# Optimization experiments

Measured on AMD Instinct MI355X. Metric: run time of the kernel, lower is better.

Reference implementation:

```python
import jax, jax.numpy as jnp
import numpy as np

N = 50000      # nodes
E = 800000     # directed edges
D = 128        # input_dim == hidden_dim
EL = 100000    # edges scored by decoder


def setup_inputs() -> dict:
    key = jax.random.key(0)
    ks = jax.random.split(key, 8)
    s = 1.0 / np.sqrt(D)  # glorot-ish scale
    return {
        "node_feature": jax.random.normal(ks[0], (N, D), jnp.float32),
        "W1": jax.random.normal(ks[1], (D, D), jnp.float32) * s,
        "b1": jnp.zeros((D,), jnp.float32),
        "W2": jax.random.normal(ks[2], (D, D), jnp.float32) * s,
        "b2": jnp.zeros((D,), jnp.float32),
        "W3": jax.random.normal(ks[3], (D, D), jnp.float32) * s,
        "b3": jnp.zeros((D,), jnp.float32),
        "edge_index": jax.random.randint(ks[4], (2, E), 0, N, dtype=jnp.int32),
        "edge_label_index": jax.random.randint(ks[5], (2, EL), 0, N, dtype=jnp.int32),
    }


def _gcn_conv(x, W, b, src, dst, norm, n):
    # x' = D^{-1/2} (A + I) D^{-1/2} (x W) + b   (PyG GCNConv semantics)
    h = x @ W                                   # [N, D]
    msg = h[src] * norm[:, None]                # gather + scale, [E+N, D]
    out = jax.ops.segment_sum(msg, dst, num_segments=n)  # scatter-add
    return out + b


def reference(node_feature, W1, b1, W2, b2, W3, b3, edge_index, edge_label_index):
    n = node_feature.shape[0]
    loop = jnp.arange(n, dtype=edge_index.dtype)
    src = jnp.concatenate([edge_index[0], loop])  # self-loops appended
    dst = jnp.concatenate([edge_index[1], loop])
    # symmetric normalization: deg over destinations (incl. self-loops)
    deg = jax.ops.segment_sum(jnp.ones_like(dst, dtype=node_feature.dtype), dst, num_segments=n)
    dinv = jax.lax.rsqrt(jnp.maximum(deg, 1.0))
    norm = dinv[src] * dinv[dst]                 # [E+N]

    x = jax.nn.relu(_gcn_conv(node_feature, W1, b1, src, dst, norm, n))
    x = jax.nn.relu(_gcn_conv(x, W2, b2, src, dst, norm, n))
    x = _gcn_conv(x, W3, b3, src, dst, norm, n)

    # dot-product edge decoder
    u = x[edge_label_index[0]]
    v = x[edge_label_index[1]]
    return jnp.sum(u * v, axis=-1)               # [EL] logits
```

## Files before the change

kernel.cpp:

```cpp
#include <hip/hip_runtime.h>
#include <hip/hip_bf16.h>
#include <hip/hip_fp16.h>

typedef _Float16 v8h __attribute__((ext_vector_type(8)));
typedef float v4f __attribute__((ext_vector_type(4)));

__global__ __launch_bounds__(256) void gemm1_deg(const float* __restrict__ X,
                                                 const float* __restrict__ W,
                                                 __half* __restrict__ H, int Nrows,
                                                 int gemmBlocks, int degBlocks,
                                                 const int* __restrict__ dst,
                                                 int* __restrict__ cnt,
                                                 int* __restrict__ rank, int E,
                                                 const float* __restrict__ W2,
                                                 const float* __restrict__ W3,
                                                 __half* __restrict__ wfrag) {
    int tid = threadIdx.x;
    if (blockIdx.x >= gemmBlocks + degBlocks) {
        int o = (blockIdx.x - gemmBlocks - degBlocks) * 256 + tid;
        int w = o >> 14, r = o & 16383;
        const float* Ws = w ? W3 : W2;
        int k = r >> 7, ncol = r & 127;
        int c = ncol >> 4, nl = ncol & 15;
        int s = k >> 5, quad = (k >> 3) & 3, j = k & 7;
        int di = ((c * 4 + s) * 64 + quad * 16 + nl) * 8 + j;
        wfrag[(size_t)w * 16384 + di] = __float2half_rn(Ws[r]);
        return;
    }
    if (blockIdx.x >= gemmBlocks) {
        int base = (blockIdx.x - gemmBlocks) * 1024 + tid * 4;
        if (base + 3 < E) {
            int d0 = dst[base], d1 = dst[base + 1], d2 = dst[base + 2], d3 = dst[base + 3];
            int r0 = atomicAdd(&cnt[d0], 1);
            int r1 = atomicAdd(&cnt[d1], 1);
            int r2 = atomicAdd(&cnt[d2], 1);
            int r3 = atomicAdd(&cnt[d3], 1);
            rank[base] = r0; rank[base + 1] = r1; rank[base + 2] = r2; rank[base + 3] = r3;
        } else {
            for (int e = base; e < E; ++e) rank[e] = atomicAdd(&cnt[dst[e]], 1);
        }
        return;
    }
    __shared__ __align__(16) float xs[16][132];
    __shared__ __align__(16) float ws[16][128];
    int tx = tid & 15;
    int ty = tid >> 4;
    int row0 = blockIdx.x * 128;
    float acc[8][8] = {};
    for (int k0 = 0; k0 < 128; k0 += 16) {
        {
            int r = tid >> 2;
            int j = (tid & 3) * 4;
            int gr = row0 + r;
            float4 v = (gr < Nrows) ? *(const float4*)&X[(size_t)gr * 128 + k0 + j]
                                    : make_float4(0.f, 0.f, 0.f, 0.f);
            xs[j + 0][r] = v.x; xs[j + 1][r] = v.y; xs[j + 2][r] = v.z; xs[j + 3][r] = v.w;
            int gr2 = gr + 64;
            float4 u = (gr2 < Nrows) ? *(const float4*)&X[(size_t)gr2 * 128 + k0 + j]
                                     : make_float4(0.f, 0.f, 0.f, 0.f);
            xs[j + 0][r + 64] = u.x; xs[j + 1][r + 64] = u.y;
            xs[j + 2][r + 64] = u.z; xs[j + 3][r + 64] = u.w;
        }
        {
            const float4* Wv = (const float4*)&W[(size_t)k0 * 128];
            float4* wsv = (float4*)&ws[0][0];
            wsv[tid] = Wv[tid];
            wsv[tid + 256] = Wv[tid + 256];
        }
        __syncthreads();
#pragma unroll
        for (int kk = 0; kk < 16; ++kk) {
            float4 xa = *(float4*)&xs[kk][ty * 4];
            float4 xb = *(float4*)&xs[kk][ty * 4 + 64];
            float4 wa = *(float4*)&ws[kk][tx * 4];
            float4 wb = *(float4*)&ws[kk][tx * 4 + 64];
            float xr[8] = {xa.x, xa.y, xa.z, xa.w, xb.x, xb.y, xb.z, xb.w};
            float wr[8] = {wa.x, wa.y, wa.z, wa.w, wb.x, wb.y, wb.z, wb.w};
#pragma unroll
            for (int i = 0; i < 8; ++i)
#pragma unroll
                for (int j = 0; j < 8; ++j)
                    acc[i][j] += xr[i] * wr[j];
        }
        __syncthreads();
    }
    auto pk = [](float x, float y) { __half2 h = __floats2half2_rn(x, y); return *(unsigned int*)&h; };
#pragma unroll
    for (int i = 0; i < 8; ++i) {
        int gr = row0 + ((i < 4) ? (ty * 4 + i) : (64 + ty * 4 + i - 4));
        if (gr < Nrows) {
            uint2 q0 = make_uint2(pk(acc[i][0], acc[i][1]), pk(acc[i][2], acc[i][3]));
            uint2 q1 = make_uint2(pk(acc[i][4], acc[i][5]), pk(acc[i][6], acc[i][7]));
            *(uint2*)&H[(size_t)gr * 128 + tx * 4] = q0;
            *(uint2*)&H[(size_t)gr * 128 + 64 + tx * 4] = q1;
        }
    }
}

__global__ __launch_bounds__(256) void agg_gemm(const __half* __restrict__ Xs,
                                                const float* __restrict__ dinv,
                                                const int* __restrict__ rowptr,
                                                const int* __restrict__ col,
                                                const __half* __restrict__ wfrag,
                                                const float* __restrict__ bias,
                                                __half* __restrict__ Out,
                                                int n, int finalLayer) {
    __shared__ __align__(16) _Float16 y[64][136];
    int tid = threadIdx.x;
    int rowbase = blockIdx.x * 64;
    {
        int sub = tid >> 4;
        int t = (tid & 15) * 8;
        for (int g = 0; g < 4; ++g) {
            int rr = g * 16 + sub;
            int node = rowbase + rr;
            float a[8] = {};
            if (node < n) {
                int beg = rowptr[node], end = rowptr[node + 1];
                int k = beg;
                for (; k + 4 <= end; k += 4) {
                    int s0 = col[k], s1 = col[k + 1], s2 = col[k + 2], s3 = col[k + 3];
                    uint4 r0 = *(const uint4*)&Xs[(size_t)s0 * 128 + t];
                    uint4 r1 = *(const uint4*)&Xs[(size_t)s1 * 128 + t];
                    uint4 r2 = *(const uint4*)&Xs[(size_t)s2 * 128 + t];
                    uint4 r3 = *(const uint4*)&Xs[(size_t)s3 * 128 + t];
                    const __half2* h0 = (const __half2*)&r0;
                    const __half2* h1 = (const __half2*)&r1;
                    const __half2* h2 = (const __half2*)&r2;
                    const __half2* h3 = (const __half2*)&r3;
#pragma unroll
                    for (int m = 0; m < 4; ++m) {
                        float2 f0 = __half22float2(h0[m]);
                        float2 f1 = __half22float2(h1[m]);
                        float2 f2 = __half22float2(h2[m]);
                        float2 f3 = __half22float2(h3[m]);
                        a[2 * m]     += (f0.x + f1.x) + (f2.x + f3.x);
                        a[2 * m + 1] += (f0.y + f1.y) + (f2.y + f3.y);
                    }
                }
                for (; k < end; ++k) {
                    uint4 r0 = *(const uint4*)&Xs[(size_t)col[k] * 128 + t];
                    const __half2* h0 = (const __half2*)&r0;
#pragma unroll
                    for (int m = 0; m < 4; ++m) {
                        float2 f0 = __half22float2(h0[m]);
                        a[2 * m] += f0.x;
                        a[2 * m + 1] += f0.y;
                    }
                }
                float dn = dinv[node];
#pragma unroll
                for (int m = 0; m < 8; ++m) a[m] *= dn;
            }
            v8h yv;
#pragma unroll
            for (int m = 0; m < 8; ++m) yv[m] = (_Float16)a[m];
            *(v8h*)&y[rr][t] = yv;
        }
    }
    __syncthreads();
    int l = tid & 63;
    int wid = tid >> 6;
    int rb = wid * 16;
    int quad = l >> 4;
    int nn = l & 15;
    v8h a0 = *(const v8h*)&y[rb + nn][0 * 32 + quad * 8];
    v8h a1 = *(const v8h*)&y[rb + nn][1 * 32 + quad * 8];
    v8h a2 = *(const v8h*)&y[rb + nn][2 * 32 + quad * 8];
    v8h a3 = *(const v8h*)&y[rb + nn][3 * 32 + quad * 8];
    const v8h* Wf = (const v8h*)wfrag;
    v4f acc[8] = {};
#pragma unroll
    for (int c = 0; c < 8; ++c) {
        v8h b0 = Wf[(c * 4 + 0) * 64 + l];
        v8h b1 = Wf[(c * 4 + 1) * 64 + l];
        v8h b2 = Wf[(c * 4 + 2) * 64 + l];
        v8h b3 = Wf[(c * 4 + 3) * 64 + l];
        acc[c] = __builtin_amdgcn_mfma_f32_16x16x32_f16(a0, b0, acc[c], 0, 0, 0);
        acc[c] = __builtin_amdgcn_mfma_f32_16x16x32_f16(a1, b1, acc[c], 0, 0, 0);
        acc[c] = __builtin_amdgcn_mfma_f32_16x16x32_f16(a2, b2, acc[c], 0, 0, 0);
        acc[c] = __builtin_amdgcn_mfma_f32_16x16x32_f16(a3, b3, acc[c], 0, 0, 0);
    }
#pragma unroll
    for (int reg = 0; reg < 4; ++reg) {
        int gr = rowbase + rb + quad * 4 + reg;
        if (gr < n) {
            float dn = dinv[gr];
#pragma unroll
            for (int c = 0; c < 8; ++c) {
                float z = acc[c][reg] + bias[c * 16 + nn];
                if (!finalLayer) z = fmaxf(z, 0.f) * dn;
                Out[(size_t)gr * 128 + c * 16 + nn] = __float2half_rn(z);
            }
        }
    }
}

__global__ void scanA(const int* __restrict__ cnt, int* __restrict__ tmp,
                      int* __restrict__ bsum, int n) {
    __shared__ int s[256];
    int i = blockIdx.x * 256 + threadIdx.x;
    int v = (i < n) ? (cnt[i] + 1) : 0;
    s[threadIdx.x] = v;
    __syncthreads();
    for (int off = 1; off < 256; off <<= 1) {
        int x = (threadIdx.x >= off) ? s[threadIdx.x - off] : 0;
        __syncthreads();
        s[threadIdx.x] += x;
        __syncthreads();
    }
    if (i < n) tmp[i] = s[threadIdx.x];
    if (threadIdx.x == 255) bsum[blockIdx.x] = s[255];
}

__global__ void scanB(const int* __restrict__ tmp, const int* __restrict__ bsum,
                      const int* __restrict__ cnt, int* __restrict__ rowptr,
                      float* __restrict__ dinv, int* __restrict__ col, int n, int nb) {
    __shared__ int p[256];
    int t = threadIdx.x;
    p[t] = (t < nb) ? bsum[t] : 0;
    __syncthreads();
    for (int off = 1; off < 256; off <<= 1) {
        int x = (t >= off) ? p[t - off] : 0;
        __syncthreads();
        p[t] += x;
        __syncthreads();
    }
    int prefix = (blockIdx.x == 0) ? 0 : p[blockIdx.x - 1];
    int i = blockIdx.x * 256 + t;
    if (i < n) {
        int inc = tmp[i] + prefix;
        rowptr[i + 1] = inc;
        int c1 = cnt[i] + 1;
        dinv[i] = rsqrtf((float)c1);
        col[inc - c1] = i;
        if (i == 0) rowptr[0] = 0;
    }
}

__global__ __launch_bounds__(256) void fill4(const int* __restrict__ src,
                                             const int* __restrict__ dst,
                                             const int* __restrict__ rank,
                                             const int* __restrict__ rowptr,
                                             int* __restrict__ col, int E) {
    int base = blockIdx.x * 1024 + threadIdx.x * 4;
    if (base + 3 < E) {
        int d0 = dst[base], d1 = dst[base + 1], d2 = dst[base + 2], d3 = dst[base + 3];
        int s0 = src[base], s1 = src[base + 1], s2 = src[base + 2], s3 = src[base + 3];
        int r0 = rank[base], r1 = rank[base + 1], r2 = rank[base + 2], r3 = rank[base + 3];
        col[rowptr[d0] + 1 + r0] = s0;
        col[rowptr[d1] + 1 + r1] = s1;
        col[rowptr[d2] + 1 + r2] = s2;
        col[rowptr[d3] + 1 + r3] = s3;
    } else {
        for (int e = base; e < E; ++e)
            col[rowptr[dst[e]] + 1 + rank[e]] = src[e];
    }
}

__global__ __launch_bounds__(256) void agg_h(const __half* __restrict__ H,
                                             const float* __restrict__ dinv,
                                             const int* __restrict__ rowptr,
                                             const int* __restrict__ col,
                                             const float* __restrict__ bias,
                                             __half* __restrict__ out, int n) {
    int node = blockIdx.x * 16 + (threadIdx.x >> 4);
    int t = (threadIdx.x & 15) * 8;
    if (node >= n) return;
    int beg = rowptr[node], end = rowptr[node + 1];
    float a[8] = {};
    int k = beg;
    for (; k + 4 <= end; k += 4) {
        int s0 = col[k], s1 = col[k + 1], s2 = col[k + 2], s3 = col[k + 3];
        float w0 = dinv[s0], w1 = dinv[s1], w2 = dinv[s2], w3 = dinv[s3];
        uint4 r0 = *(const uint4*)&H[(size_t)s0 * 128 + t];
        uint4 r1 = *(const uint4*)&H[(size_t)s1 * 128 + t];
        uint4 r2 = *(const uint4*)&H[(size_t)s2 * 128 + t];
        uint4 r3 = *(const uint4*)&H[(size_t)s3 * 128 + t];
        const __half2* h0 = (const __half2*)&r0;
        const __half2* h1 = (const __half2*)&r1;
        const __half2* h2 = (const __half2*)&r2;
        const __half2* h3 = (const __half2*)&r3;
#pragma unroll
        for (int m = 0; m < 4; ++m) {
            float2 f0 = __half22float2(h0[m]);
            float2 f1 = __half22float2(h1[m]);
            float2 f2 = __half22float2(h2[m]);
            float2 f3 = __half22float2(h3[m]);
            a[2 * m]     += f0.x * w0 + f1.x * w1 + f2.x * w2 + f3.x * w3;
            a[2 * m + 1] += f0.y * w0 + f1.y * w1 + f2.y * w2 + f3.y * w3;
        }
    }
    for (; k < end; ++k) {
        int s0 = col[k];
        float w0 = dinv[s0];
        uint4 r0 = *(const uint4*)&H[(size_t)s0 * 128 + t];
        const __half2* h0 = (const __half2*)&r0;
#pragma unroll
        for (int m = 0; m < 4; ++m) {
            float2 f0 = __half22float2(h0[m]);
            a[2 * m] += f0.x * w0;
            a[2 * m + 1] += f0.y * w0;
        }
    }
    float dn = dinv[node];
    float4 b0 = *(const float4*)&bias[t];
    float4 b1 = *(const float4*)&bias[t + 4];
    float r0 = fmaxf(a[0] * dn + b0.x, 0.f) * dn;
    float r1 = fmaxf(a[1] * dn + b0.y, 0.f) * dn;
    float r2 = fmaxf(a[2] * dn + b0.z, 0.f) * dn;
    float r3 = fmaxf(a[3] * dn + b0.w, 0.f) * dn;
    float r4 = fmaxf(a[4] * dn + b1.x, 0.f) * dn;
    float r5 = fmaxf(a[5] * dn + b1.y, 0.f) * dn;
    float r6 = fmaxf(a[6] * dn + b1.z, 0.f) * dn;
    float r7 = fmaxf(a[7] * dn + b1.w, 0.f) * dn;
    auto pk = [](float x, float y) { __half2 h = __floats2half2_rn(x, y); return *(unsigned int*)&h; };
    uint4 o = make_uint4(pk(r0, r1), pk(r2, r3), pk(r4, r5), pk(r6, r7));
    *(uint4*)&out[(size_t)node * 128 + t] = o;
}

__global__ __launch_bounds__(256) void decoder_h(const __half* __restrict__ X,
                                                 const int* __restrict__ eli,
                                                 float* __restrict__ out, int EL) {
    int e = blockIdx.x * 16 + (threadIdx.x >> 4);
    int lane = threadIdx.x & 15;
    if (e >= EL) return;
    int u = eli[e], v = eli[EL + e];
    uint4 ra = *(const uint4*)&X[(size_t)u * 128 + lane * 8];
    uint4 rb = *(const uint4*)&X[(size_t)v * 128 + lane * 8];
    const __half2* ha = (const __half2*)&ra;
    const __half2* hb = (const __half2*)&rb;
    float d = 0.f;
#pragma unroll
    for (int j = 0; j < 4; ++j) {
        float2 fa = __half22float2(ha[j]);
        float2 fb = __half22float2(hb[j]);
        d += fa.x * fb.x + fa.y * fb.y;
    }
#pragma unroll
    for (int off = 8; off > 0; off >>= 1) d += __shfl_xor(d, off);
    if (lane == 0) out[e] = d;
}

extern "C" void kernel_launch(void* const* d_in, const int* in_sizes, int n_in,
                              void* d_out, int out_size, void* d_ws, size_t ws_size,
                              hipStream_t stream) {
    const float* x0 = (const float*)d_in[0];
    const float* W1 = (const float*)d_in[1];
    const float* b1 = (const float*)d_in[2];
    const float* W2 = (const float*)d_in[3];
    const float* b2 = (const float*)d_in[4];
    const float* W3 = (const float*)d_in[5];
    const float* b3 = (const float*)d_in[6];
    const int* ei   = (const int*)d_in[7];
    const int* eli  = (const int*)d_in[8];
    float* out = (float*)d_out;

    const int D = 128;
    const int N  = in_sizes[0] / D;
    const int E  = in_sizes[7] / 2;
    const int EL = in_sizes[8] / 2;

    const int* src = ei;
    const int* dst = ei + E;

    char* ws = (char*)d_ws;
    size_t off = 0;
    auto alloc = [&](size_t bytes) -> void* {
        off = (off + 255) & ~(size_t)255;
        void* p = ws + off;
        off += bytes;
        return p;
    };
    int*    cnt    = (int*)alloc((size_t)N * sizeof(int));
    int*    tmp    = (int*)alloc((size_t)N * sizeof(int));
    int*    bsum   = (int*)alloc(256 * sizeof(int));
    int*    rowptr = (int*)alloc((size_t)(N + 1) * sizeof(int));
    float*  dinv   = (float*)alloc((size_t)N * sizeof(float));
    int*    rank   = (int*)alloc((size_t)E * sizeof(int));
    int*    col    = (int*)alloc((size_t)(E + N) * sizeof(int));
    __half* wfrag  = (__half*)alloc((size_t)2 * 16384 * sizeof(__half));
    __half* hbuf   = (__half*)alloc((size_t)N * D * sizeof(__half));
    __half* xbuf   = (__half*)alloc((size_t)N * D * sizeof(__half));
    (void)ws_size;

    hipMemsetAsync(cnt, 0, (size_t)N * sizeof(int), stream);

    int nbN = (N + 255) / 256;
    int nbE4 = (E + 1023) / 1024;
    int gemmGrid = (N + 127) / 128;
    int fusedGrid = (N + 63) / 64;
    int aggGrid  = (N + 15) / 16;

    gemm1_deg<<<gemmGrid + nbE4 + 128, 256, 0, stream>>>(x0, W1, hbuf, N,
                                                         gemmGrid, nbE4,
                                                         dst, cnt, rank, E,
                                                         W2, W3, wfrag);

    scanA<<<nbN, 256, 0, stream>>>(cnt, tmp, bsum, N);
    scanB<<<nbN, 256, 0, stream>>>(tmp, bsum, cnt, rowptr, dinv, col, N, nbN);
    fill4<<<nbE4, 256, 0, stream>>>(src, dst, rank, rowptr, col, E);

    agg_h<<<aggGrid, 256, 0, stream>>>(hbuf, dinv, rowptr, col, b1, xbuf, N);
    agg_gemm<<<fusedGrid, 256, 0, stream>>>(xbuf, dinv, rowptr, col, wfrag, b2, hbuf, N, 0);
    agg_gemm<<<fusedGrid, 256, 0, stream>>>(hbuf, dinv, rowptr, col, wfrag + 16384, b3, xbuf, N, 1);

    decoder_h<<<(EL + 15) / 16, 256, 0, stream>>>(xbuf, eli, out, EL);
}
```

Measured before the change: 271.3 us.

## Replace first-layer FP32 GEMM with fp16 convert and aggregate-then-MFMA layer

New measurement: 275.3 us. Within noise of the previous version (+1.5%).

```diff
diff --git a/kernel.cpp b/kernel.cpp
--- a/kernel.cpp
+++ b/kernel.cpp
@@ -5,21 +5,33 @@
 typedef _Float16 v8h __attribute__((ext_vector_type(8)));
 typedef float v4f __attribute__((ext_vector_type(4)));
 
-__global__ __launch_bounds__(256) void gemm1_deg(const float* __restrict__ X,
-                                                 const float* __restrict__ W,
-                                                 __half* __restrict__ H, int Nrows,
-                                                 int gemmBlocks, int degBlocks,
-                                                 const int* __restrict__ dst,
-                                                 int* __restrict__ cnt,
-                                                 int* __restrict__ rank, int E,
-                                                 const float* __restrict__ W2,
-                                                 const float* __restrict__ W3,
-                                                 __half* __restrict__ wfrag) {
+__global__ __launch_bounds__(256) void conv_swz_deg(const float* __restrict__ X0,
+                                                    __half* __restrict__ Xh, int nElem8,
+                                                    int convBlocks,
+                                                    const float* __restrict__ W1,
+                                                    const float* __restrict__ W2,
+                                                    const float* __restrict__ W3,
+                                                    __half* __restrict__ wfrag,
+                                                    const int* __restrict__ dst,
+                                                    int* __restrict__ cnt,
+                                                    int* __restrict__ rank, int E) {
     int tid = threadIdx.x;
-    if (blockIdx.x >= gemmBlocks + degBlocks) {
-        int o = (blockIdx.x - gemmBlocks - degBlocks) * 256 + tid;
+    if (blockIdx.x < convBlocks) {
+        int i = blockIdx.x * 256 + tid;
+        if (i < nElem8) {
+            float4 v0 = ((const float4*)X0)[i * 2];
+            float4 v1 = ((const float4*)X0)[i * 2 + 1];
+            auto pk = [](float x, float y) { __half2 h = __floats2half2_rn(x, y); return *(unsigned int*)&h; };
+            uint4 q = make_uint4(pk(v0.x, v0.y), pk(v0.z, v0.w), pk(v1.x, v1.y), pk(v1.z, v1.w));
+            ((uint4*)Xh)[i] = q;
+        }
+        return;
+    }
+    int bb = blockIdx.x - convBlocks;
+    if (bb < 192) {
+        int o = bb * 256 + tid;
         int w = o >> 14, r = o & 16383;
-        const float* Ws = w ? W3 : W2;
+        const float* Ws = (w == 0) ? W1 : (w == 1) ? W2 : W3;
         int k = r >> 7, ncol = r & 127;
         int c = ncol >> 4, nl = ncol & 15;
         int s = k >> 5, quad = (k >> 3) & 3, j = k & 7;
@@ -27,172 +39,16 @@
         wfrag[(size_t)w * 16384 + di] = __float2half_rn(Ws[r]);
         return;
     }
-    if (blockIdx.x >= gemmBlocks) {
-        int base = (blockIdx.x - gemmBlocks) * 1024 + tid * 4;
-        if (base + 3 < E) {
-            int d0 = dst[base], d1 = dst[base + 1], d2 = dst[base + 2], d3 = dst[base + 3];
-            int r0 = atomicAdd(&cnt[d0], 1);
-            int r1 = atomicAdd(&cnt[d1], 1);
-            int r2 = atomicAdd(&cnt[d2], 1);
-            int r3 = atomicAdd(&cnt[d3], 1);
-            rank[base] = r0; rank[base + 1] = r1; rank[base + 2] = r2; rank[base + 3] = r3;
-        } else {
-            for (int e = base; e < E; ++e) rank[e] = atomicAdd(&cnt[dst[e]], 1);
-        }
-        return;
-    }
-    __shared__ __align__(16) float xs[16][132];
-    __shared__ __align__(16) float ws[16][128];
-    int tx = tid & 15;
-    int ty = tid >> 4;
-    int row0 = blockIdx.x * 128;
-    float acc[8][8] = {};
-    for (int k0 = 0; k0 < 128; k0 += 16) {
-        {
-            int r = tid >> 2;
-            int j = (tid & 3) * 4;
-            int gr = row0 + r;
-            float4 v = (gr < Nrows) ? *(const float4*)&X[(size_t)gr * 128 + k0 + j]
-                                    : make_float4(0.f, 0.f, 0.f, 0.f);
-            xs[j + 0][r] = v.x; xs[j + 1][r] = v.y; xs[j + 2][r] = v.z; xs[j + 3][r] = v.w;
-            int gr2 = gr + 64;
-            float4 u = (gr2 < Nrows) ? *(const float4*)&X[(size_t)gr2 * 128 + k0 + j]
-                                     : make_float4(0.f, 0.f, 0.f, 0.f);
-            xs[j + 0][r + 64] = u.x; xs[j + 1][r + 64] = u.y;
-            xs[j + 2][r + 64] = u.z; xs[j + 3][r + 64] = u.w;
-        }
-        {
-            const float4* Wv = (const float4*)&W[(size_t)k0 * 128];
-            float4* wsv = (float4*)&ws[0][0];
-            wsv[tid] = Wv[tid];
-            wsv[tid + 256] = Wv[tid + 256];
-        }
-        __syncthreads();
-#pragma unroll
-        for (int kk = 0; kk < 16; ++kk) {
-            float4 xa = *(float4*)&xs[kk][ty * 4];
-            float4 xb = *(float4*)&xs[kk][ty * 4 + 64];
-            float4 wa = *(float4*)&ws[kk][tx * 4];
-            float4 wb = *(float4*)&ws[kk][tx * 4 + 64];
-            float xr[8] = {xa.x, xa.y, xa.z, xa.w, xb.x, xb.y, xb.z, xb.w};
-            float wr[8] = {wa.x, wa.y, wa.z, wa.w, wb.x, wb.y, wb.z, wb.w};
-#pragma unroll
-            for (int i = 0; i < 8; ++i)
-#pragma unroll
-                for (int j = 0; j < 8; ++j)
-                    acc[i][j] += xr[i] * wr[j];
-        }
-        __syncthreads();
-    }
-    auto pk = [](float x, float y) { __half2 h = __floats2half2_rn(x, y); return *(unsigned int*)&h; };
-#pragma unroll
-    for (int i = 0; i < 8; ++i) {
-        int gr = row0 + ((i < 4) ? (ty * 4 + i) : (64 + ty * 4 + i - 4));
-        if (gr < Nrows) {
-            uint2 q0 = make_uint2(pk(acc[i][0], acc[i][1]), pk(acc[i][2], acc[i][3]));
-            uint2 q1 = make_uint2(pk(acc[i][4], acc[i][5]), pk(acc[i][6], acc[i][7]));
-            *(uint2*)&H[(size_t)gr * 128 + tx * 4] = q0;
-            *(uint2*)&H[(size_t)gr * 128 + 64 + tx * 4] = q1;
-        }
-    }
-}
-
-__global__ __launch_bounds__(256) void agg_gemm(const __half* __restrict__ Xs,
-                                                const float* __restrict__ dinv,
-                                                const int* __restrict__ rowptr,
-                                                const int* __restrict__ col,
-                                                const __half* __restrict__ wfrag,
-                                                const float* __restrict__ bias,
-                                                __half* __restrict__ Out,
-                                                int n, int finalLayer) {
-    __shared__ __align__(16) _Float16 y[64][136];
-    int tid = threadIdx.x;
-    int rowbase = blockIdx.x * 64;
-    {
-        int sub = tid >> 4;
-        int t = (tid & 15) * 8;
-        for (int g = 0; g < 4; ++g) {
-            int rr = g * 16 + sub;
-            int node = rowbase + rr;
-            float a[8] = {};
-            if (node < n) {
-                int beg = rowptr[node], end = rowptr[node + 1];
-                int k = beg;
-                for (; k + 4 <= end; k += 4) {
-                    int s0 = col[k], s1 = col[k + 1], s2 = col[k + 2], s3 = col[k + 3];
-                    uint4 r0 = *(const uint4*)&Xs[(size_t)s0 * 128 + t];
-                    uint4 r1 = *(const uint4*)&Xs[(size_t)s1 * 128 + t];
-                    uint4 r2 = *(const uint4*)&Xs[(size_t)s2 * 128 + t];
-                    uint4 r3 = *(const uint4*)&Xs[(size_t)s3 * 128 + t];
-                    const __half2* h0 = (const __half2*)&r0;
-                    const __half2* h1 = (const __half2*)&r1;
-                    const __half2* h2 = (const __half2*)&r2;
-                    const __half2* h3 = (const __half2*)&r3;
-#pragma unroll
-                    for (int m = 0; m < 4; ++m) {
-                        float2 f0 = __half22float2(h0[m]);
-                        float2 f1 = __half22float2(h1[m]);
-                        float2 f2 = __half22float2(h2[m]);
-                        float2 f3 = __half22float2(h3[m]);
-                        a[2 * m]     += (f0.x + f1.x) + (f2.x + f3.x);
-                        a[2 * m + 1] += (f0.y + f1.y) + (f2.y + f3.y);
-                    }
-                }
-                for (; k < end; ++k) {
-                    uint4 r0 = *(const uint4*)&Xs[(size_t)col[k] * 128 + t];
-                    const __half2* h0 = (const __half2*)&r0;
-#pragma unroll
-                    for (int m = 0; m < 4; ++m) {
-                        float2 f0 = __half22float2(h0[m]);
-                        a[2 * m] += f0.x;
-                        a[2 * m + 1] += f0.y;
-                    }
-                }
-                float dn = dinv[node];
-#pragma unroll
-                for (int m = 0; m < 8; ++m) a[m] *= dn;
-            }
-            v8h yv;
-#pragma unroll
-            for (int m = 0; m < 8; ++m) yv[m] = (_Float16)a[m];
-            *(v8h*)&y[rr][t] = yv;
-        }
-    }
-    __syncthreads();
-    int l = tid & 63;
-    int wid = tid >> 6;
-    int rb = wid * 16;
-    int quad = l >> 4;
-    int nn = l & 15;
-    v8h a0 = *(const v8h*)&y[rb + nn][0 * 32 + quad * 8];
-    v8h a1 = *(const v8h*)&y[rb + nn][1 * 32 + quad * 8];
-    v8h a2 = *(const v8h*)&y[rb + nn][2 * 32 + quad * 8];
-    v8h a3 = *(const v8h*)&y[rb + nn][3 * 32 + quad * 8];
-    const v8h* Wf = (const v8h*)wfrag;
-    v4f acc[8] = {};
-#pragma unroll
-    for (int c = 0; c < 8; ++c) {
-        v8h b0 = Wf[(c * 4 + 0) * 64 + l];
-        v8h b1 = Wf[(c * 4 + 1) * 64 + l];
-        v8h b2 = Wf[(c * 4 + 2) * 64 + l];
-        v8h b3 = Wf[(c * 4 + 3) * 64 + l];
-        acc[c] = __builtin_amdgcn_mfma_f32_16x16x32_f16(a0, b0, acc[c], 0, 0, 0);
-        acc[c] = __builtin_amdgcn_mfma_f32_16x16x32_f16(a1, b1, acc[c], 0, 0, 0);
-        acc[c] = __builtin_amdgcn_mfma_f32_16x16x32_f16(a2, b2, acc[c], 0, 0, 0);
-        acc[c] = __builtin_amdgcn_mfma_f32_16x16x32_f16(a3, b3, acc[c], 0, 0, 0);
-    }
-#pragma unroll
-    for (int reg = 0; reg < 4; ++reg) {
-        int gr = rowbase + rb + quad * 4 + reg;
-        if (gr < n) {
-            float dn = dinv[gr];
-#pragma unroll
-            for (int c = 0; c < 8; ++c) {
-                float z = acc[c][reg] + bias[c * 16 + nn];
-                if (!finalLayer) z = fmaxf(z, 0.f) * dn;
-                Out[(size_t)gr * 128 + c * 16 + nn] = __float2half_rn(z);
-            }
-        }
+    int base = (bb - 192) * 1024 + tid * 4;
+    if (base + 3 < E) {
+        int d0 = dst[base], d1 = dst[base + 1], d2 = dst[base + 2], d3 = dst[base + 3];
+        int r0 = atomicAdd(&cnt[d0], 1);
+        int r1 = atomicAdd(&cnt[d1], 1);
+        int r2 = atomicAdd(&cnt[d2], 1);
+        int r3 = atomicAdd(&cnt[d3], 1);
+        rank[base] = r0; rank[base + 1] = r1; rank[base + 2] = r2; rank[base + 3] = r3;
+    } else {
+        for (int e = base; e < E; ++e) rank[e] = atomicAdd(&cnt[dst[e]], 1);
     }
 }
 
@@ -258,65 +114,107 @@
     }
 }
 
-__global__ __launch_bounds__(256) void agg_h(const __half* __restrict__ H,
-                                             const float* __restrict__ dinv,
-                                             const int* __restrict__ rowptr,
-                                             const int* __restrict__ col,
-                                             const float* __restrict__ bias,
-                                             __half* __restrict__ out, int n) {
-    int node = blockIdx.x * 16 + (threadIdx.x >> 4);
-    int t = (threadIdx.x & 15) * 8;
-    if (node >= n) return;
-    int beg = rowptr[node], end = rowptr[node + 1];
-    float a[8] = {};
-    int k = beg;
-    for (; k + 4 <= end; k += 4) {
-        int s0 = col[k], s1 = col[k + 1], s2 = col[k + 2], s3 = col[k + 3];
-        float w0 = dinv[s0], w1 = dinv[s1], w2 = dinv[s2], w3 = dinv[s3];
-        uint4 r0 = *(const uint4*)&H[(size_t)s0 * 128 + t];
-        uint4 r1 = *(const uint4*)&H[(size_t)s1 * 128 + t];
-        uint4 r2 = *(const uint4*)&H[(size_t)s2 * 128 + t];
-        uint4 r3 = *(const uint4*)&H[(size_t)s3 * 128 + t];
-        const __half2* h0 = (const __half2*)&r0;
-        const __half2* h1 = (const __half2*)&r1;
-        const __half2* h2 = (const __half2*)&r2;
-        const __half2* h3 = (const __half2*)&r3;
-#pragma unroll
-        for (int m = 0; m < 4; ++m) {
-            float2 f0 = __half22float2(h0[m]);
-            float2 f1 = __half22float2(h1[m]);
-            float2 f2 = __half22float2(h2[m]);
-            float2 f3 = __half22float2(h3[m]);
-            a[2 * m]     += f0.x * w0 + f1.x * w1 + f2.x * w2 + f3.x * w3;
-            a[2 * m + 1] += f0.y * w0 + f1.y * w1 + f2.y * w2 + f3.y * w3;
+__global__ __launch_bounds__(256) void agg_gemm(const __half* __restrict__ Xs,
+                                                const float* __restrict__ dinv,
+                                                const int* __restrict__ rowptr,
+                                                const int* __restrict__ col,
+                                                const __half* __restrict__ wfrag,
+                                                const float* __restrict__ bias,
+                                                __half* __restrict__ Out,
+                                                int n, int finalLayer, int gdinv) {
+    __shared__ __align__(16) _Float16 y[64][136];
+    int tid = threadIdx.x;
+    int rowbase = blockIdx.x * 64;
+    {
+        int sub = tid >> 4;
+        int t = (tid & 15) * 8;
+        for (int g = 0; g < 4; ++g) {
+            int rr = g * 16 + sub;
+            int node = rowbase + rr;
+            float a[8] = {};
+            if (node < n) {
+                int beg = rowptr[node], end = rowptr[node + 1];
+                int k = beg;
+                for (; k + 4 <= end; k += 4) {
+                    int s0 = col[k], s1 = col[k + 1], s2 = col[k + 2], s3 = col[k + 3];
+                    float w0 = 1.f, w1 = 1.f, w2 = 1.f, w3 = 1.f;
+                    if (gdinv) { w0 = dinv[s0]; w1 = dinv[s1]; w2 = dinv[s2]; w3 = dinv[s3]; }
+                    uint4 r0 = *(const uint4*)&Xs[(size_t)s0 * 128 + t];
+                    uint4 r1 = *(const uint4*)&Xs[(size_t)s1 * 128 + t];
+                    uint4 r2 = *(const uint4*)&Xs[(size_t)s2 * 128 + t];
+                    uint4 r3 = *(const uint4*)&Xs[(size_t)s3 * 128 + t];
+                    const __half2* h0 = (const __half2*)&r0;
+                    const __half2* h1 = (const __half2*)&r1;
+                    const __half2* h2 = (const __half2*)&r2;
+                    const __half2* h3 = (const __half2*)&r3;
+#pragma unroll
+                    for (int m = 0; m < 4; ++m) {
+                        float2 f0 = __half22float2(h0[m]);
+                        float2 f1 = __half22float2(h1[m]);
+                        float2 f2 = __half22float2(h2[m]);
+                        float2 f3 = __half22float2(h3[m]);
+                        a[2 * m]     += f0.x * w0 + f1.x * w1 + f2.x * w2 + f3.x * w3;
+                        a[2 * m + 1] += f0.y * w0 + f1.y * w1 + f2.y * w2 + f3.y * w3;
+                    }
+                }
+                for (; k < end; ++k) {
+                    int s0 = col[k];
+                    float w0 = gdinv ? dinv[s0] : 1.f;
+                    uint4 r0 = *(const uint4*)&Xs[(size_t)s0 * 128 + t];
+                    const __half2* h0 = (const __half2*)&r0;
+#pragma unroll
+                    for (int m = 0; m < 4; ++m) {
+                        float2 f0 = __half22float2(h0[m]);
+                        a[2 * m] += f0.x * w0;
+                        a[2 * m + 1] += f0.y * w0;
+                    }
+                }
+                float dn = dinv[node];
+#pragma unroll
+                for (int m = 0; m < 8; ++m) a[m] *= dn;
+            }
+            v8h yv;
+#pragma unroll
+            for (int m = 0; m < 8; ++m) yv[m] = (_Float16)a[m];
+            *(v8h*)&y[rr][t] = yv;
         }
     }
-    for (; k < end; ++k) {
-        int s0 = col[k];
-        float w0 = dinv[s0];
-        uint4 r0 = *(const uint4*)&H[(size_t)s0 * 128 + t];
-        const __half2* h0 = (const __half2*)&r0;
-#pragma unroll
-        for (int m = 0; m < 4; ++m) {
-            float2 f0 = __half22float2(h0[m]);
-            a[2 * m] += f0.x * w0;
-            a[2 * m + 1] += f0.y * w0;
+    __syncthreads();
+    int l = tid & 63;
+    int wid = tid >> 6;
+    int rb = wid * 16;
+    int quad = l >> 4;
+    int nn = l & 15;
+    v8h a0 = *(const v8h*)&y[rb + nn][0 * 32 + quad * 8];
+    v8h a1 = *(const v8h*)&y[rb + nn][1 * 32 + quad * 8];
+    v8h a2 = *(const v8h*)&y[rb + nn][2 * 32 + quad * 8];
+    v8h a3 = *(const v8h*)&y[rb + nn][3 * 32 + quad * 8];
+    const v8h* Wf = (const v8h*)wfrag;
+    v4f acc[8] = {};
+#pragma unroll
+    for (int c = 0; c < 8; ++c) {
+        v8h b0 = Wf[(c * 4 + 0) * 64 + l];
+        v8h b1 = Wf[(c * 4 + 1) * 64 + l];
+        v8h b2 = Wf[(c * 4 + 2) * 64 + l];
+        v8h b3 = Wf[(c * 4 + 3) * 64 + l];
+        acc[c] = __builtin_amdgcn_mfma_f32_16x16x32_f16(a0, b0, acc[c], 0, 0, 0);
+        acc[c] = __builtin_amdgcn_mfma_f32_16x16x32_f16(a1, b1, acc[c], 0, 0, 0);
+        acc[c] = __builtin_amdgcn_mfma_f32_16x16x32_f16(a2, b2, acc[c], 0, 0, 0);
+        acc[c] = __builtin_amdgcn_mfma_f32_16x16x32_f16(a3, b3, acc[c], 0, 0, 0);
+    }
+#pragma unroll
+    for (int reg = 0; reg < 4; ++reg) {
+        int gr = rowbase + rb + quad * 4 + reg;
+        if (gr < n) {
+            float dn = dinv[gr];
+#pragma unroll
+            for (int c = 0; c < 8; ++c) {
+                float z = acc[c][reg] + bias[c * 16 + nn];
+                if (!finalLayer) z = fmaxf(z, 0.f) * dn;
+                Out[(size_t)gr * 128 + c * 16 + nn] = __float2half_rn(z);
+            }
         }
     }
-    float dn = dinv[node];
-    float4 b0 = *(const float4*)&bias[t];
-    float4 b1 = *(const float4*)&bias[t + 4];
-    float r0 = fmaxf(a[0] * dn + b0.x, 0.f) * dn;
-    float r1 = fmaxf(a[1] * dn + b0.y, 0.f) * dn;
-    float r2 = fmaxf(a[2] * dn + b0.z, 0.f) * dn;
-    float r3 = fmaxf(a[3] * dn + b0.w, 0.f) * dn;
-    float r4 = fmaxf(a[4] * dn + b1.x, 0.f) * dn;
-    float r5 = fmaxf(a[5] * dn + b1.y, 0.f) * dn;
-    float r6 = fmaxf(a[6] * dn + b1.z, 0.f) * dn;
-    float r7 = fmaxf(a[7] * dn + b1.w, 0.f) * dn;
-    auto pk = [](float x, float y) { __half2 h = __floats2half2_rn(x, y); return *(unsigned int*)&h; };
-    uint4 o = make_uint4(pk(r0, r1), pk(r2, r3), pk(r4, r5), pk(r6, r7));
-    *(uint4*)&out[(size_t)node * 128 + t] = o;
 }
 
 __global__ __launch_bounds__(256) void decoder_h(const __half* __restrict__ X,
@@ -379,7 +277,8 @@
     float*  dinv   = (float*)alloc((size_t)N * sizeof(float));
     int*    rank   = (int*)alloc((size_t)E * sizeof(int));
     int*    col    = (int*)alloc((size_t)(E + N) * sizeof(int));
-    __half* wfrag  = (__half*)alloc((size_t)2 * 16384 * sizeof(__half));
+    __half* wfrag  = (__half*)alloc((size_t)3 * 16384 * sizeof(__half));
+    __half* xh0    = (__half*)alloc((size_t)N * D * sizeof(__half));
     __half* hbuf   = (__half*)alloc((size_t)N * D * sizeof(__half));
     __half* xbuf   = (__half*)alloc((size_t)N * D * sizeof(__half));
     (void)ws_size;
@@ -388,22 +287,21 @@
 
     int nbN = (N + 255) / 256;
     int nbE4 = (E + 1023) / 1024;
-    int gemmGrid = (N + 127) / 128;
     int fusedGrid = (N + 63) / 64;
-    int aggGrid  = (N + 15) / 16;
-
-    gemm1_deg<<<gemmGrid + nbE4 + 128, 256, 0, stream>>>(x0, W1, hbuf, N,
-                                                         gemmGrid, nbE4,
-                                                         dst, cnt, rank, E,
-                                                         W2, W3, wfrag);
+    int nElem8    = N * D / 8;
+    int convBlocks = (nElem8 + 255) / 256;
+
+    conv_swz_deg<<<convBlocks + 192 + nbE4, 256, 0, stream>>>(x0, xh0, nElem8, convBlocks,
+                                                              W1, W2, W3, wfrag,
+                                                              dst, cnt, rank, E);
 
     scanA<<<nbN, 256, 0, stream>>>(cnt, tmp, bsum, N);
     scanB<<<nbN, 256, 0, stream>>>(tmp, bsum, cnt, rowptr, dinv, col, N, nbN);
     fill4<<<nbE4, 256, 0, stream>>>(src, dst, rank, rowptr, col, E);
 
-    agg_h<<<aggGrid, 256, 0, stream>>>(hbuf, dinv, rowptr, col, b1, xbuf, N);
-    agg_gemm<<<fusedGrid, 256, 0, stream>>>(xbuf, dinv, rowptr, col, wfrag, b2, hbuf, N, 0);
-    agg_gemm<<<fusedGrid, 256, 0, stream>>>(hbuf, dinv, rowptr, col, wfrag + 16384, b3, xbuf, N, 1);
-
-    decoder_h<<<(EL + 15) / 16, 256, 0, stream>>>(xbuf, eli, out, EL);
-}
+    agg_gemm<<<fusedGrid, 256, 0, stream>>>(xh0, dinv, rowptr, col, wfrag, b1, hbuf, N, 0, 1);
+    agg_gemm<<<fusedGrid, 256, 0, stream>>>(hbuf, dinv, rowptr, col, wfrag + 16384, b2, xbuf, N, 0, 0);
+    agg_gemm<<<fusedGrid, 256, 0, stream>>>(xbuf, dinv, rowptr, col, wfrag + 2 * 16384, b3, hbuf, N, 1, 0);
+
+    decoder_h<<<(EL + 15) / 16, 256, 0, stream>>>(hbuf, eli, out, EL);
+}
```
